# Kernel tuning notes

Measured on AMD Instinct MI355X. Metric: run time of the kernel, lower is better.

The kernel has to match this reference:

```python
import jax, jax.numpy as jnp
import numpy as np

N_USERS = 100000
N_ITEMS = 40000
DIM = 64
NNZ_UI = 1500000
NNZ_II = 1000000
NNZ_UU = 1500000
UI_LAYERS = 3
ITEM_LAYERS = 2
USER_LAYERS = 2
EPS = 1e-12


def spmm(rows, cols, vals, x, n_rows):
    # sparse COO matrix (rows, cols, vals) @ dense x -> [n_rows, d]
    return jax.ops.segment_sum(vals[:, None] * x[cols], rows, num_segments=n_rows)


def l2_normalize(x):
    # matches F.normalize(x, p=2, dim=1) with eps clamp
    n = jnp.linalg.norm(x, axis=1, keepdims=True)
    return x / jnp.maximum(n, EPS)


def setup_inputs() -> dict:
    key = jax.random.key(0)
    ks = jax.random.split(key, 13)
    N = N_USERS + N_ITEMS
    return {
        "user_ui_emb": jax.random.normal(ks[0], (N_USERS, DIM), jnp.float32) * 0.1,
        "item_ui_emb": jax.random.normal(ks[1], (N_ITEMS, DIM), jnp.float32) * 0.1,
        "uu_emb": jax.random.normal(ks[2], (N_USERS, DIM), jnp.float32) * 0.1,
        "ii_emb": jax.random.normal(ks[3], (N_ITEMS, DIM), jnp.float32) * 0.1,
        "ui_vals": jax.random.uniform(ks[4], (NNZ_UI,), jnp.float32) / 12.0,
        "ii_vals": jax.random.uniform(ks[5], (NNZ_II,), jnp.float32) / 25.0,
        "uu_vals": jax.random.uniform(ks[6], (NNZ_UU,), jnp.float32) / 15.0,
        "ui_rows": jax.random.randint(ks[7], (NNZ_UI,), 0, N, jnp.int32),
        "ui_cols": jax.random.randint(ks[8], (NNZ_UI,), 0, N, jnp.int32),
        "ii_rows": jax.random.randint(ks[9], (NNZ_II,), 0, N_ITEMS, jnp.int32),
        "ii_cols": jax.random.randint(ks[10], (NNZ_II,), 0, N_ITEMS, jnp.int32),
        "uu_rows": jax.random.randint(ks[11], (NNZ_UU,), 0, N_USERS, jnp.int32),
        "uu_cols": jax.random.randint(ks[12], (NNZ_UU,), 0, N_USERS, jnp.int32),
    }


def reference(user_ui_emb, item_ui_emb, uu_emb, ii_emb,
              ui_vals, ii_vals, uu_vals,
              ui_rows, ui_cols, ii_rows, ii_cols, uu_rows, uu_cols):
    N = N_USERS + N_ITEMS
    # II propagation (item_loss_ratio != 0)
    ii = ii_emb
    for _ in range(ITEM_LAYERS):
        ii = spmm(ii_rows, ii_cols, ii_vals, ii, N_ITEMS)
    # UU propagation (user_loss_ratio != 0)
    uu = uu_emb
    for _ in range(USER_LAYERS):
        uu = spmm(uu_rows, uu_cols, uu_vals, uu, N_USERS)
    # LightGCN UI propagation
    ego = jnp.concatenate([user_ui_emb, item_ui_emb], axis=0)  # [N, d]
    acc = ego
    for _ in range(UI_LAYERS):
        ego = spmm(ui_rows, ui_cols, ui_vals, ego, N)
        acc = acc + ego
    all_emb = acc / (UI_LAYERS + 1)  # mean over stacked layers
    u_ui_emb = all_emb[:N_USERS]
    i_ui_emb = all_emb[N_USERS:]
    i_ui_emb = i_ui_emb + l2_normalize(ii)
    u_ui_emb = u_ui_emb + l2_normalize(uu)
    return (u_ui_emb, i_ui_emb, ii, uu)
```

## Files before the change

### kernel.cpp

```cpp
#include <hip/hip_runtime.h>

#define N_USERS_C 100000
#define N_ITEMS_C 40000
#define NTOT_C    140000
#define DIM_C     64

__device__ __forceinline__ unsigned short f2bf(float f) {
    unsigned u = __float_as_uint(f);
    unsigned r = (u + 0x7FFFu + ((u >> 16) & 1u)) >> 16;
    return (unsigned short)r;
}
__device__ __forceinline__ float bf2f(unsigned short h) {
    return __uint_as_float((unsigned)h << 16);
}


template <int LOG_BR>
__global__ __launch_bounds__(256) void bucket_hist(
    const int* __restrict__ rows, int* __restrict__ bkt_count, int nnz, int NB) {
    __shared__ int cnt[256];
    if (threadIdx.x < NB) cnt[threadIdx.x] = 0;
    __syncthreads();
    for (int e = blockIdx.x * 256 + threadIdx.x; e < nnz; e += gridDim.x * 256)
        atomicAdd(&cnt[rows[e] >> LOG_BR], 1);
    __syncthreads();
    if (threadIdx.x < NB) {
        int c = cnt[threadIdx.x];
        if (c) atomicAdd(&bkt_count[threadIdx.x], c);
    }
}

__global__ __launch_bounds__(256) void bucket_scan(
    const int* __restrict__ bkt_count, int* __restrict__ bkt_start,
    int* __restrict__ bkt_cursor, int NB, int nnz) {
    __shared__ int s[256];
    int v = (threadIdx.x < NB) ? bkt_count[threadIdx.x] : 0;
    s[threadIdx.x] = v;
    __syncthreads();
    #pragma unroll
    for (int off = 1; off < 256; off <<= 1) {
        int t = (threadIdx.x >= off) ? s[threadIdx.x - off] : 0;
        __syncthreads();
        s[threadIdx.x] += t;
        __syncthreads();
    }
    if (threadIdx.x < NB) {
        int ex = s[threadIdx.x] - v;
        bkt_start[threadIdx.x] = ex;
        bkt_cursor[threadIdx.x] = ex;
    }
    if (threadIdx.x == 0) bkt_start[NB] = nnz;
}

template <int LOG_BR>
__global__ __launch_bounds__(256) void partition_edges(
    const int* __restrict__ rows, const int* __restrict__ cols,
    const float* __restrict__ vals, int* __restrict__ bkt_cursor,
    int2* __restrict__ inter, int nnz) {
    __shared__ int cnt[256];
    __shared__ int base[256];
    const int tile = blockIdx.x * 4096;
    cnt[threadIdx.x] = 0;
    __syncthreads();
    int myrow[16];
    #pragma unroll
    for (int i = 0; i < 16; ++i) {
        int e = tile + i * 256 + threadIdx.x;
        int r = (e < nnz) ? rows[e] : -1;
        myrow[i] = r;
        if (r >= 0) atomicAdd(&cnt[r >> LOG_BR], 1);
    }
    __syncthreads();
    {
        int c = cnt[threadIdx.x];
        if (c) base[threadIdx.x] = atomicAdd(&bkt_cursor[threadIdx.x], c);
        cnt[threadIdx.x] = 0;
    }
    __syncthreads();
    #pragma unroll
    for (int i = 0; i < 16; ++i) {
        int r = myrow[i];
        if (r < 0) continue;
        int b = r >> LOG_BR;
        int rank = atomicAdd(&cnt[b], 1);
        int e = tile + i * 256 + threadIdx.x;
        int rl = r & ((1 << LOG_BR) - 1);
        inter[base[b] + rank] = make_int2((rl << 18) | cols[e],
                                          __float_as_int(vals[e]));
    }
}

template <int LOG_BR>
__global__ __launch_bounds__(256) void bucket_to_csr(
    const int* __restrict__ bkt_start, const int2* __restrict__ inter,
    int2* __restrict__ spack, int* __restrict__ rowptr, int n_rows, int nnz) {
    const int BR = 1 << LOG_BR;
    const int C = BR / 256;
    __shared__ int hist[BR];
    __shared__ int bsum[256];
    const int b = blockIdx.x;
    const int lo = bkt_start[b], hi = bkt_start[b + 1];
    #pragma unroll
    for (int j = 0; j < C; ++j) hist[threadIdx.x * C + j] = 0;
    __syncthreads();
    for (int i = lo + threadIdx.x; i < hi; i += 256)
        atomicAdd(&hist[inter[i].x >> 18], 1);
    __syncthreads();
    int loc[4];
    int sum = 0;
    #pragma unroll
    for (int j = 0; j < C; ++j) { loc[j] = sum; sum += hist[threadIdx.x * C + j]; }
    bsum[threadIdx.x] = sum;
    __syncthreads();
    #pragma unroll
    for (int off = 1; off < 256; off <<= 1) {
        int t = (threadIdx.x >= off) ? bsum[threadIdx.x - off] : 0;
        __syncthreads();
        bsum[threadIdx.x] += t;
        __syncthreads();
    }
    int texcl = bsum[threadIdx.x] - sum;
    __syncthreads();
    #pragma unroll
    for (int j = 0; j < C; ++j) {
        int r = threadIdx.x * C + j;
        int abs0 = lo + texcl + loc[j];
        int grow = (b << LOG_BR) + r;
        if (grow < n_rows) rowptr[grow] = abs0;
        hist[r] = abs0;
    }
    if (b == gridDim.x - 1 && threadIdx.x == 0) rowptr[n_rows] = nnz;
    __syncthreads();
    for (int i = lo + threadIdx.x; i < hi; i += 256) {
        int2 p = inter[i];
        int pos = atomicAdd(&hist[p.x >> 18], 1);
        spack[pos] = make_int2(p.x & 0x3FFFF, p.y);
    }
}

__global__ __launch_bounds__(256) void to_bf16(
    const float* __restrict__ src, unsigned short* __restrict__ dst, int n4) {
    int gid = blockIdx.x * blockDim.x + threadIdx.x;
    if (gid >= n4) return;
    float4 v = ((const float4*)src)[gid];
    ushort4 o;
    o.x = f2bf(v.x); o.y = f2bf(v.y); o.z = f2bf(v.z); o.w = f2bf(v.w);
    ((ushort4*)dst)[gid] = o;
}

__global__ __launch_bounds__(256) void concat_to_bf16(
    const float* __restrict__ user_ui, const float* __restrict__ item_ui,
    unsigned short* __restrict__ dst) {
    int gid = blockIdx.x * blockDim.x + threadIdx.x;
    const int n4u = N_USERS_C * DIM_C / 4;
    const int n4  = NTOT_C * DIM_C / 4;
    if (gid >= n4) return;
    float4 v = (gid < n4u) ? ((const float4*)user_ui)[gid]
                           : ((const float4*)item_ui)[gid - n4u];
    ushort4 o;
    o.x = f2bf(v.x); o.y = f2bf(v.y); o.z = f2bf(v.z); o.w = f2bf(v.w);
    ((ushort4*)dst)[gid] = o;
}

template <int MODE>
__global__ __launch_bounds__(256) void spmm_csr2(
    const int* __restrict__ rowptr, const int2* __restrict__ spack,
    const unsigned short* __restrict__ x, unsigned short* __restrict__ out_bf,
    float* __restrict__ out_f32, float* __restrict__ acc,
    const float* __restrict__ ego_u, const float* __restrict__ ego_i,
    int n_rows, int nnz) {
    const int wpair = (blockIdx.x * 256 + threadIdx.x) >> 6;
    const int lane  = threadIdx.x & 63;
    const int l     = lane & 31;
    const int row   = wpair * 2 + (lane >> 5);

    int j = rowptr[row];
    int e = rowptr[row + 1];
    int rem = e - j;
    int orem = __shfl_xor(rem, 32, 64);
    int mrem = rem > orem ? rem : orem;

    const unsigned* __restrict__ xw = (const unsigned*)x;
    const int last = nnz - 1;

    float s0x = 0.f, s0y = 0.f, s1x = 0.f, s1y = 0.f;
    float s2x = 0.f, s2y = 0.f, s3x = 0.f, s3y = 0.f;

    if (mrem > 0) {
        int base = j;
        int2 p0 = spack[min(base + 0, last)];
        int2 p1 = spack[min(base + 1, last)];
        int2 p2 = spack[min(base + 2, last)];
        int2 p3 = spack[min(base + 3, last)];
        for (;;) {
            unsigned g0 = xw[(0 < rem) ? ((p0.x << 5) + l) : l];
            unsigned g1 = xw[(1 < rem) ? ((p1.x << 5) + l) : l];
            unsigned g2 = xw[(2 < rem) ? ((p2.x << 5) + l) : l];
            unsigned g3 = xw[(3 < rem) ? ((p3.x << 5) + l) : l];
            int nb = base + 4;
            int2 q0 = spack[min(nb + 0, last)];
            int2 q1 = spack[min(nb + 1, last)];
            int2 q2 = spack[min(nb + 2, last)];
            int2 q3 = spack[min(nb + 3, last)];
            float v0 = (0 < rem) ? __int_as_float(p0.y) : 0.f;
            float v1 = (1 < rem) ? __int_as_float(p1.y) : 0.f;
            float v2 = (2 < rem) ? __int_as_float(p2.y) : 0.f;
            float v3 = (3 < rem) ? __int_as_float(p3.y) : 0.f;
            s0x += v0 * __uint_as_float(g0 << 16);
            s0y += v0 * __uint_as_float(g0 & 0xFFFF0000u);
            s1x += v1 * __uint_as_float(g1 << 16);
            s1y += v1 * __uint_as_float(g1 & 0xFFFF0000u);
            s2x += v2 * __uint_as_float(g2 << 16);
            s2y += v2 * __uint_as_float(g2 & 0xFFFF0000u);
            s3x += v3 * __uint_as_float(g3 << 16);
            s3y += v3 * __uint_as_float(g3 & 0xFFFF0000u);
            mrem -= 4;
            if (mrem <= 0) break;
            rem -= 4;
            base = nb;
            p0 = q0; p1 = q1; p2 = q2; p3 = q3;
        }
    }
    float sx = (s0x + s1x) + (s2x + s3x);
    float sy = (s0y + s1y) + (s2y + s3y);

    const size_t idx2 = (size_t)row * 32 + l;
    if (MODE == 0 || MODE == 1 || MODE == 2) {
        ushort2 o;
        o.x = f2bf(sx);
        o.y = f2bf(sy);
        ((ushort2*)out_bf)[idx2] = o;
    }
    if (MODE == 1) {
        float2 e2 = (row < N_USERS_C)
            ? ((const float2*)ego_u)[idx2]
            : ((const float2*)ego_i)[(size_t)(row - N_USERS_C) * 32 + l];
        ((float2*)acc)[idx2] = make_float2(e2.x + sx, e2.y + sy);
    } else if (MODE == 2 || MODE == 3) {
        float2 a = ((float2*)acc)[idx2];
        ((float2*)acc)[idx2] = make_float2(a.x + sx, a.y + sy);
    } else if (MODE == 4) {
        ((float2*)out_f32)[idx2] = make_float2(sx, sy);
        float ss = sx * sx + sy * sy;
        #pragma unroll
        for (int off = 1; off < 32; off <<= 1) ss += __shfl_xor(ss, off, 64);
        float denom = fmaxf(sqrtf(ss), 1e-12f);
        float2 a = ((float2*)acc)[idx2];
        a.x = a.x * 0.25f + sx / denom;
        a.y = a.y * 0.25f + sy / denom;
        ((float2*)acc)[idx2] = a;
    }
}


struct BuildWs {
    int2* spack;
    int2* inter;
    int* rowptr;
    int* bkt_count;
    int* bkt_start;
    int* bkt_cursor;
};

template <int LOG_BR>
static inline void build_csr(const int* rows, const int* cols, const float* vals,
                             int nnz, int n_rows, const BuildWs& W, hipStream_t s) {
    const int NB = (n_rows + (1 << LOG_BR) - 1) >> LOG_BR;
    hipMemsetAsync(W.bkt_count, 0, (size_t)NB * sizeof(int), s);
    bucket_hist<LOG_BR><<<512, 256, 0, s>>>(rows, W.bkt_count, nnz, NB);
    bucket_scan<<<1, 256, 0, s>>>(W.bkt_count, W.bkt_start, W.bkt_cursor, NB, nnz);
    int p1b = (nnz + 4095) / 4096;
    partition_edges<LOG_BR><<<p1b, 256, 0, s>>>(rows, cols, vals, W.bkt_cursor,
                                                W.inter, nnz);
    bucket_to_csr<LOG_BR><<<NB, 256, 0, s>>>(W.bkt_start, W.inter, W.spack,
                                             W.rowptr, n_rows, nnz);
}

template <int MODE>
static inline void run_spmm(const int* rowptr, const int2* spack,
                            const unsigned short* x, unsigned short* out_bf,
                            float* out_f32, float* acc, const float* ego_u,
                            const float* ego_i, int n_rows, int nnz, hipStream_t s) {
    int blocks = (n_rows * 32 + 255) / 256;
    spmm_csr2<MODE><<<blocks, 256, 0, s>>>(rowptr, spack, x, out_bf, out_f32,
                                           acc, ego_u, ego_i, n_rows, nnz);
}

extern "C" void kernel_launch(void* const* d_in, const int* in_sizes, int n_in,
                              void* d_out, int out_size, void* d_ws, size_t ws_size,
                              hipStream_t stream) {
    const float* user_ui = (const float*)d_in[0];
    const float* item_ui = (const float*)d_in[1];
    const float* uu_emb  = (const float*)d_in[2];
    const float* ii_emb  = (const float*)d_in[3];
    const float* ui_vals = (const float*)d_in[4];
    const float* ii_vals = (const float*)d_in[5];
    const float* uu_vals = (const float*)d_in[6];
    const int* ui_rows = (const int*)d_in[7];
    const int* ui_cols = (const int*)d_in[8];
    const int* ii_rows = (const int*)d_in[9];
    const int* ii_cols = (const int*)d_in[10];
    const int* uu_rows = (const int*)d_in[11];
    const int* uu_cols = (const int*)d_in[12];
    const int nnz_ui = in_sizes[4];
    const int nnz_ii = in_sizes[5];
    const int nnz_uu = in_sizes[6];
    const int max_nnz = nnz_ui > nnz_uu ? (nnz_ui > nnz_ii ? nnz_ui : nnz_ii)
                                        : (nnz_uu > nnz_ii ? nnz_uu : nnz_ii);

    float* out    = (float*)d_out;
    float* acc    = out;
    float* acc_u  = acc;
    float* acc_i  = acc + (size_t)N_USERS_C * DIM_C;
    float* out_ii = out + (size_t)NTOT_C * DIM_C;
    float* out_uu = out_ii + (size_t)N_ITEMS_C * DIM_C;

    char* p = (char*)d_ws;
    BuildWs W;
    W.spack = (int2*)p;                         p += (size_t)max_nnz * sizeof(int2);
    unsigned short* buf0 = (unsigned short*)p;
    W.inter = (int2*)p;                         p += (size_t)NTOT_C * DIM_C * sizeof(unsigned short);
    unsigned short* buf1 = (unsigned short*)p;  p += (size_t)NTOT_C * DIM_C * sizeof(unsigned short);
    W.rowptr     = (int*)p;                     p += (size_t)(NTOT_C + 1) * sizeof(int);
    W.bkt_count  = (int*)p;                     p += 257 * sizeof(int);
    W.bkt_start  = (int*)p;                     p += 258 * sizeof(int);
    W.bkt_cursor = (int*)p;                     p += 257 * sizeof(int);

    build_csr<10>(ui_rows, ui_cols, ui_vals, nnz_ui, NTOT_C, W, stream);
    {
        int n4 = NTOT_C * DIM_C / 4;
        concat_to_bf16<<<(n4 + 255) / 256, 256, 0, stream>>>(user_ui, item_ui, buf1);
    }
    run_spmm<1>(W.rowptr, W.spack, buf1, buf0, nullptr, acc, user_ui, item_ui,
                NTOT_C, nnz_ui, stream);
    run_spmm<2>(W.rowptr, W.spack, buf0, buf1, nullptr, acc, nullptr, nullptr,
                NTOT_C, nnz_ui, stream);
    run_spmm<3>(W.rowptr, W.spack, buf1, nullptr, nullptr, acc, nullptr, nullptr,
                NTOT_C, nnz_ui, stream);

    build_csr<8>(ii_rows, ii_cols, ii_vals, nnz_ii, N_ITEMS_C, W, stream);
    {
        int n4 = N_ITEMS_C * DIM_C / 4;
        to_bf16<<<(n4 + 255) / 256, 256, 0, stream>>>(ii_emb, buf0, n4);
    }
    run_spmm<0>(W.rowptr, W.spack, buf0, buf1, nullptr, nullptr, nullptr, nullptr,
                N_ITEMS_C, nnz_ii, stream);
    run_spmm<4>(W.rowptr, W.spack, buf1, nullptr, out_ii, acc_i, nullptr, nullptr,
                N_ITEMS_C, nnz_ii, stream);

    build_csr<9>(uu_rows, uu_cols, uu_vals, nnz_uu, N_USERS_C, W, stream);
    {
        int n4 = N_USERS_C * DIM_C / 4;
        to_bf16<<<(n4 + 255) / 256, 256, 0, stream>>>(uu_emb, buf0, n4);
    }
    run_spmm<0>(W.rowptr, W.spack, buf0, buf1, nullptr, nullptr, nullptr, nullptr,
                N_USERS_C, nnz_uu, stream);
    run_spmm<4>(W.rowptr, W.spack, buf1, nullptr, out_uu, acc_u, nullptr, nullptr,
                N_USERS_C, nnz_uu, stream);
}
```

Before: 712.1 us.

## Batch II and UU graphs into one block-diagonal CSR; use quarter-wave rows

The separate item-item and user-user propagations are merged into one block-diagonal sparse matrix over a concatenated embedding, with row and column offsets applied during partitioning. This halves the number of CSR builds and SpMM launches for those graphs, and MODE 5 remaps rows back into the accumulator. The SpMM kernel also changes from 32 lanes per row with 2 bf16 values each to 16 lanes per row with 4 values each, so a wave handles 4 rows and issues wider gathers. The fallback keeps the separate path when the workspace is too small, and the grid size now assumes n_rows is divisible by 16.

```diff
diff --git a/kernel.cpp b/kernel.cpp
--- a/kernel.cpp
+++ b/kernel.cpp
@@ -10,19 +10,17 @@
     unsigned r = (u + 0x7FFFu + ((u >> 16) & 1u)) >> 16;
     return (unsigned short)r;
 }
-__device__ __forceinline__ float bf2f(unsigned short h) {
-    return __uint_as_float((unsigned)h << 16);
-}
 
 
 template <int LOG_BR>
 __global__ __launch_bounds__(256) void bucket_hist(
-    const int* __restrict__ rows, int* __restrict__ bkt_count, int nnz, int NB) {
+    const int* __restrict__ rows, int row_off, int* __restrict__ bkt_count,
+    int nnz, int NB) {
     __shared__ int cnt[256];
     if (threadIdx.x < NB) cnt[threadIdx.x] = 0;
     __syncthreads();
     for (int e = blockIdx.x * 256 + threadIdx.x; e < nnz; e += gridDim.x * 256)
-        atomicAdd(&cnt[rows[e] >> LOG_BR], 1);
+        atomicAdd(&cnt[(rows[e] + row_off) >> LOG_BR], 1);
     __syncthreads();
     if (threadIdx.x < NB) {
         int c = cnt[threadIdx.x];
@@ -55,8 +53,8 @@
 template <int LOG_BR>
 __global__ __launch_bounds__(256) void partition_edges(
     const int* __restrict__ rows, const int* __restrict__ cols,
-    const float* __restrict__ vals, int* __restrict__ bkt_cursor,
-    int2* __restrict__ inter, int nnz) {
+    const float* __restrict__ vals, int row_off, int col_off,
+    int* __restrict__ bkt_cursor, int2* __restrict__ inter, int nnz) {
     __shared__ int cnt[256];
     __shared__ int base[256];
     const int tile = blockIdx.x * 4096;
@@ -66,7 +64,7 @@
     #pragma unroll
     for (int i = 0; i < 16; ++i) {
         int e = tile + i * 256 + threadIdx.x;
-        int r = (e < nnz) ? rows[e] : -1;
+        int r = (e < nnz) ? (rows[e] + row_off) : -1;
         myrow[i] = r;
         if (r >= 0) atomicAdd(&cnt[r >> LOG_BR], 1);
     }
@@ -85,7 +83,7 @@
         int rank = atomicAdd(&cnt[b], 1);
         int e = tile + i * 256 + threadIdx.x;
         int rl = r & ((1 << LOG_BR) - 1);
-        inter[base[b] + rank] = make_int2((rl << 18) | cols[e],
+        inter[base[b] + rank] = make_int2((rl << 18) | (cols[e] + col_off),
                                           __float_as_int(vals[e]));
     }
 }
@@ -138,152 +136,122 @@
     }
 }
 
-__global__ __launch_bounds__(256) void to_bf16(
-    const float* __restrict__ src, unsigned short* __restrict__ dst, int n4) {
+__global__ __launch_bounds__(256) void concat2_to_bf16(
+    const float* __restrict__ A, const float* __restrict__ B, int n4A,
+    int n4tot, unsigned short* __restrict__ dst) {
     int gid = blockIdx.x * blockDim.x + threadIdx.x;
-    if (gid >= n4) return;
-    float4 v = ((const float4*)src)[gid];
+    if (gid >= n4tot) return;
+    float4 v = (gid < n4A) ? ((const float4*)A)[gid] : ((const float4*)B)[gid - n4A];
     ushort4 o;
     o.x = f2bf(v.x); o.y = f2bf(v.y); o.z = f2bf(v.z); o.w = f2bf(v.w);
     ((ushort4*)dst)[gid] = o;
 }
 
-__global__ __launch_bounds__(256) void concat_to_bf16(
-    const float* __restrict__ user_ui, const float* __restrict__ item_ui,
-    unsigned short* __restrict__ dst) {
-    int gid = blockIdx.x * blockDim.x + threadIdx.x;
-    const int n4u = N_USERS_C * DIM_C / 4;
-    const int n4  = NTOT_C * DIM_C / 4;
-    if (gid >= n4) return;
-    float4 v = (gid < n4u) ? ((const float4*)user_ui)[gid]
-                           : ((const float4*)item_ui)[gid - n4u];
-    ushort4 o;
-    o.x = f2bf(v.x); o.y = f2bf(v.y); o.z = f2bf(v.z); o.w = f2bf(v.w);
-    ((ushort4*)dst)[gid] = o;
-}
-
 template <int MODE>
-__global__ __launch_bounds__(256) void spmm_csr2(
+__global__ __launch_bounds__(256) void spmm_csr4(
     const int* __restrict__ rowptr, const int2* __restrict__ spack,
     const unsigned short* __restrict__ x, unsigned short* __restrict__ out_bf,
     float* __restrict__ out_f32, float* __restrict__ acc,
     const float* __restrict__ ego_u, const float* __restrict__ ego_i,
     int n_rows, int nnz) {
-    const int wpair = (blockIdx.x * 256 + threadIdx.x) >> 6;
-    const int lane  = threadIdx.x & 63;
-    const int l     = lane & 31;
-    const int row   = wpair * 2 + (lane >> 5);
+    const int wq   = (blockIdx.x * 256 + threadIdx.x) >> 6;
+    const int lane = threadIdx.x & 63;
+    const int l    = lane & 15;
+    const int row  = wq * 4 + (lane >> 4);
 
     int j = rowptr[row];
     int e = rowptr[row + 1];
     int rem = e - j;
-    int orem = __shfl_xor(rem, 32, 64);
-    int mrem = rem > orem ? rem : orem;
-
-    const unsigned* __restrict__ xw = (const unsigned*)x;
+    int m1 = max(rem, __shfl_xor(rem, 16, 64));
+    int mrem = max(m1, __shfl_xor(m1, 32, 64));
+
+    const uint2* __restrict__ xq = (const uint2*)x;
     const int last = nnz - 1;
 
-    float s0x = 0.f, s0y = 0.f, s1x = 0.f, s1y = 0.f;
-    float s2x = 0.f, s2y = 0.f, s3x = 0.f, s3y = 0.f;
+    float4 sa[4];
+    #pragma unroll
+    for (int u = 0; u < 4; ++u) sa[u] = make_float4(0.f, 0.f, 0.f, 0.f);
 
     if (mrem > 0) {
         int base = j;
-        int2 p0 = spack[min(base + 0, last)];
-        int2 p1 = spack[min(base + 1, last)];
-        int2 p2 = spack[min(base + 2, last)];
-        int2 p3 = spack[min(base + 3, last)];
+        int2 p[4];
+        #pragma unroll
+        for (int u = 0; u < 4; ++u) p[u] = spack[min(base + u, last)];
         for (;;) {
-            unsigned g0 = xw[(0 < rem) ? ((p0.x << 5) + l) : l];
-            unsigned g1 = xw[(1 < rem) ? ((p1.x << 5) + l) : l];
-            unsigned g2 = xw[(2 < rem) ? ((p2.x << 5) + l) : l];
-            unsigned g3 = xw[(3 < rem) ? ((p3.x << 5) + l) : l];
+            uint2 g[4];
+            #pragma unroll
+            for (int u = 0; u < 4; ++u)
+                g[u] = xq[(u < rem) ? ((p[u].x << 4) + l) : l];
             int nb = base + 4;
-            int2 q0 = spack[min(nb + 0, last)];
-            int2 q1 = spack[min(nb + 1, last)];
-            int2 q2 = spack[min(nb + 2, last)];
-            int2 q3 = spack[min(nb + 3, last)];
-            float v0 = (0 < rem) ? __int_as_float(p0.y) : 0.f;
-            float v1 = (1 < rem) ? __int_as_float(p1.y) : 0.f;
-            float v2 = (2 < rem) ? __int_as_float(p2.y) : 0.f;
-            float v3 = (3 < rem) ? __int_as_float(p3.y) : 0.f;
-            s0x += v0 * __uint_as_float(g0 << 16);
-            s0y += v0 * __uint_as_float(g0 & 0xFFFF0000u);
-            s1x += v1 * __uint_as_float(g1 << 16);
-            s1y += v1 * __uint_as_float(g1 & 0xFFFF0000u);
-            s2x += v2 * __uint_as_float(g2 << 16);
-            s2y += v2 * __uint_as_float(g2 & 0xFFFF0000u);
-            s3x += v3 * __uint_as_float(g3 << 16);
-            s3y += v3 * __uint_as_float(g3 & 0xFFFF0000u);
+            int2 q[4];
+            #pragma unroll
+            for (int u = 0; u < 4; ++u) q[u] = spack[min(nb + u, last)];
+            #pragma unroll
+            for (int u = 0; u < 4; ++u) {
+                float v = (u < rem) ? __int_as_float(p[u].y) : 0.f;
+                sa[u].x += v * __uint_as_float(g[u].x << 16);
+                sa[u].y += v * __uint_as_float(g[u].x & 0xFFFF0000u);
+                sa[u].z += v * __uint_as_float(g[u].y << 16);
+                sa[u].w += v * __uint_as_float(g[u].y & 0xFFFF0000u);
+            }
             mrem -= 4;
             if (mrem <= 0) break;
             rem -= 4;
             base = nb;
-            p0 = q0; p1 = q1; p2 = q2; p3 = q3;
+            #pragma unroll
+            for (int u = 0; u < 4; ++u) p[u] = q[u];
         }
     }
-    float sx = (s0x + s1x) + (s2x + s3x);
-    float sy = (s0y + s1y) + (s2y + s3y);
-
-    const size_t idx2 = (size_t)row * 32 + l;
+    float4 s;
+    s.x = (sa[0].x + sa[1].x) + (sa[2].x + sa[3].x);
+    s.y = (sa[0].y + sa[1].y) + (sa[2].y + sa[3].y);
+    s.z = (sa[0].z + sa[1].z) + (sa[2].z + sa[3].z);
+    s.w = (sa[0].w + sa[1].w) + (sa[2].w + sa[3].w);
+
+    const size_t idx4 = (size_t)row * 16 + l;
     if (MODE == 0 || MODE == 1 || MODE == 2) {
-        ushort2 o;
-        o.x = f2bf(sx);
-        o.y = f2bf(sy);
-        ((ushort2*)out_bf)[idx2] = o;
+        ushort4 o;
+        o.x = f2bf(s.x); o.y = f2bf(s.y); o.z = f2bf(s.z); o.w = f2bf(s.w);
+        ((ushort4*)out_bf)[idx4] = o;
     }
     if (MODE == 1) {
-        float2 e2 = (row < N_USERS_C)
-            ? ((const float2*)ego_u)[idx2]
-            : ((const float2*)ego_i)[(size_t)(row - N_USERS_C) * 32 + l];
-        ((float2*)acc)[idx2] = make_float2(e2.x + sx, e2.y + sy);
+        float4 e4 = (row < N_USERS_C)
+            ? ((const float4*)ego_u)[idx4]
+            : ((const float4*)ego_i)[(size_t)(row - N_USERS_C) * 16 + l];
+        ((float4*)acc)[idx4] = make_float4(e4.x + s.x, e4.y + s.y,
+                                           e4.z + s.z, e4.w + s.w);
     } else if (MODE == 2 || MODE == 3) {
-        float2 a = ((float2*)acc)[idx2];
-        ((float2*)acc)[idx2] = make_float2(a.x + sx, a.y + sy);
-    } else if (MODE == 4) {
-        ((float2*)out_f32)[idx2] = make_float2(sx, sy);
-        float ss = sx * sx + sy * sy;
+        float4 a = ((const float4*)acc)[idx4];
+        ((float4*)acc)[idx4] = make_float4(a.x + s.x, a.y + s.y,
+                                           a.z + s.z, a.w + s.w);
+    } else if (MODE == 4 || MODE == 5) {
+        ((float4*)out_f32)[idx4] = s;
+        float ss = s.x * s.x + s.y * s.y + s.z * s.z + s.w * s.w;
         #pragma unroll
-        for (int off = 1; off < 32; off <<= 1) ss += __shfl_xor(ss, off, 64);
-        float denom = fmaxf(sqrtf(ss), 1e-12f);
-        float2 a = ((float2*)acc)[idx2];
-        a.x = a.x * 0.25f + sx / denom;
-        a.y = a.y * 0.25f + sy / denom;
-        ((float2*)acc)[idx2] = a;
-    }
-}
-
-
-struct BuildWs {
-    int2* spack;
-    int2* inter;
-    int* rowptr;
-    int* bkt_count;
-    int* bkt_start;
-    int* bkt_cursor;
-};
-
-template <int LOG_BR>
-static inline void build_csr(const int* rows, const int* cols, const float* vals,
-                             int nnz, int n_rows, const BuildWs& W, hipStream_t s) {
-    const int NB = (n_rows + (1 << LOG_BR) - 1) >> LOG_BR;
-    hipMemsetAsync(W.bkt_count, 0, (size_t)NB * sizeof(int), s);
-    bucket_hist<LOG_BR><<<512, 256, 0, s>>>(rows, W.bkt_count, nnz, NB);
-    bucket_scan<<<1, 256, 0, s>>>(W.bkt_count, W.bkt_start, W.bkt_cursor, NB, nnz);
-    int p1b = (nnz + 4095) / 4096;
-    partition_edges<LOG_BR><<<p1b, 256, 0, s>>>(rows, cols, vals, W.bkt_cursor,
-                                                W.inter, nnz);
-    bucket_to_csr<LOG_BR><<<NB, 256, 0, s>>>(W.bkt_start, W.inter, W.spack,
-                                             W.rowptr, n_rows, nnz);
-}
+        for (int off = 1; off < 16; off <<= 1) ss += __shfl_xor(ss, off, 64);
+        float inv = 1.f / fmaxf(sqrtf(ss), 1e-12f);
+        size_t aidx = idx4;
+        if (MODE == 5) {
+            int arow = (row < N_ITEMS_C) ? (N_USERS_C + row) : (row - N_ITEMS_C);
+            aidx = (size_t)arow * 16 + l;
+        }
+        float4 a = ((const float4*)acc)[aidx];
+        a.x = a.x * 0.25f + s.x * inv;
+        a.y = a.y * 0.25f + s.y * inv;
+        a.z = a.z * 0.25f + s.z * inv;
+        a.w = a.w * 0.25f + s.w * inv;
+        ((float4*)acc)[aidx] = a;
+    }
+}
+
 
 template <int MODE>
 static inline void run_spmm(const int* rowptr, const int2* spack,
                             const unsigned short* x, unsigned short* out_bf,
                             float* out_f32, float* acc, const float* ego_u,
                             const float* ego_i, int n_rows, int nnz, hipStream_t s) {
-    int blocks = (n_rows * 32 + 255) / 256;
-    spmm_csr2<MODE><<<blocks, 256, 0, s>>>(rowptr, spack, x, out_bf, out_f32,
-                                           acc, ego_u, ego_i, n_rows, nnz);
+    spmm_csr4<MODE><<<n_rows / 16, 256, 0, s>>>(rowptr, spack, x, out_bf, out_f32,
+                                                acc, ego_u, ego_i, n_rows, nnz);
 }
 
 extern "C" void kernel_launch(void* const* d_in, const int* in_sizes, int n_in,
@@ -305,8 +273,7 @@
     const int nnz_ui = in_sizes[4];
     const int nnz_ii = in_sizes[5];
     const int nnz_uu = in_sizes[6];
-    const int max_nnz = nnz_ui > nnz_uu ? (nnz_ui > nnz_ii ? nnz_ui : nnz_ii)
-                                        : (nnz_uu > nnz_ii ? nnz_uu : nnz_ii);
+    const int nnz_cat = nnz_ii + nnz_uu;
 
     float* out    = (float*)d_out;
     float* acc    = out;
@@ -314,47 +281,112 @@
     float* acc_i  = acc + (size_t)N_USERS_C * DIM_C;
     float* out_ii = out + (size_t)NTOT_C * DIM_C;
     float* out_uu = out_ii + (size_t)N_ITEMS_C * DIM_C;
+    float* out_cat = out_ii;
+
+    const size_t buf_bytes = (size_t)NTOT_C * DIM_C * sizeof(unsigned short);
+    const size_t sp_ui  = (size_t)nnz_ui * sizeof(int2);
+    const size_t sp_cat = (size_t)nnz_cat * sizeof(int2);
+    const size_t meta_bytes = ((size_t)(NTOT_C + 1) + 1024) * sizeof(int);
+
+    size_t slotA = sp_cat > sp_ui ? sp_cat : sp_ui;
+    size_t slotB = slotA > buf_bytes ? slotA : buf_bytes;
+    bool use_cat = ws_size >= slotA + slotB + buf_bytes + meta_bytes;
+    if (!use_cat) {
+        size_t mx = sp_ui;
+        if ((size_t)nnz_ii * sizeof(int2) > mx) mx = (size_t)nnz_ii * sizeof(int2);
+        if ((size_t)nnz_uu * sizeof(int2) > mx) mx = (size_t)nnz_uu * sizeof(int2);
+        slotA = mx;
+        slotB = buf_bytes;
+    }
 
     char* p = (char*)d_ws;
-    BuildWs W;
-    W.spack = (int2*)p;                         p += (size_t)max_nnz * sizeof(int2);
-    unsigned short* buf0 = (unsigned short*)p;
-    W.inter = (int2*)p;                         p += (size_t)NTOT_C * DIM_C * sizeof(unsigned short);
-    unsigned short* buf1 = (unsigned short*)p;  p += (size_t)NTOT_C * DIM_C * sizeof(unsigned short);
-    W.rowptr     = (int*)p;                     p += (size_t)(NTOT_C + 1) * sizeof(int);
-    W.bkt_count  = (int*)p;                     p += 257 * sizeof(int);
-    W.bkt_start  = (int*)p;                     p += 258 * sizeof(int);
-    W.bkt_cursor = (int*)p;                     p += 257 * sizeof(int);
-
-    build_csr<10>(ui_rows, ui_cols, ui_vals, nnz_ui, NTOT_C, W, stream);
+    int2* spack = (int2*)p;                     p += slotA;
+    int2* inter = (int2*)p;
+    unsigned short* buf0 = (unsigned short*)p;  p += slotB;
+    unsigned short* buf1 = (unsigned short*)p;  p += buf_bytes;
+    int* rowptr     = (int*)p;
+    int* bkt_count  = rowptr + (NTOT_C + 1);
+    int* bkt_start  = bkt_count + 257;
+    int* bkt_cursor = bkt_start + 258;
+
+    const int n4tot = NTOT_C * DIM_C / 4;
+    const int n4u   = N_USERS_C * DIM_C / 4;
+    const int n4i   = N_ITEMS_C * DIM_C / 4;
+
     {
-        int n4 = NTOT_C * DIM_C / 4;
-        concat_to_bf16<<<(n4 + 255) / 256, 256, 0, stream>>>(user_ui, item_ui, buf1);
-    }
-    run_spmm<1>(W.rowptr, W.spack, buf1, buf0, nullptr, acc, user_ui, item_ui,
+        const int NB = (NTOT_C + 1023) >> 10;
+        hipMemsetAsync(bkt_count, 0, (size_t)NB * sizeof(int), stream);
+        bucket_hist<10><<<512, 256, 0, stream>>>(ui_rows, 0, bkt_count, nnz_ui, NB);
+        bucket_scan<<<1, 256, 0, stream>>>(bkt_count, bkt_start, bkt_cursor, NB, nnz_ui);
+        partition_edges<10><<<(nnz_ui + 4095) / 4096, 256, 0, stream>>>(
+            ui_rows, ui_cols, ui_vals, 0, 0, bkt_cursor, inter, nnz_ui);
+        bucket_to_csr<10><<<NB, 256, 0, stream>>>(bkt_start, inter, spack, rowptr,
+                                                  NTOT_C, nnz_ui);
+    }
+    concat2_to_bf16<<<(n4tot + 255) / 256, 256, 0, stream>>>(user_ui, item_ui,
+                                                             n4u, n4tot, buf1);
+    run_spmm<1>(rowptr, spack, buf1, buf0, nullptr, acc, user_ui, item_ui,
                 NTOT_C, nnz_ui, stream);
-    run_spmm<2>(W.rowptr, W.spack, buf0, buf1, nullptr, acc, nullptr, nullptr,
+    run_spmm<2>(rowptr, spack, buf0, buf1, nullptr, acc, nullptr, nullptr,
                 NTOT_C, nnz_ui, stream);
-    run_spmm<3>(W.rowptr, W.spack, buf1, nullptr, nullptr, acc, nullptr, nullptr,
+    run_spmm<3>(rowptr, spack, buf1, nullptr, nullptr, acc, nullptr, nullptr,
                 NTOT_C, nnz_ui, stream);
 
-    build_csr<8>(ii_rows, ii_cols, ii_vals, nnz_ii, N_ITEMS_C, W, stream);
-    {
-        int n4 = N_ITEMS_C * DIM_C / 4;
-        to_bf16<<<(n4 + 255) / 256, 256, 0, stream>>>(ii_emb, buf0, n4);
-    }
-    run_spmm<0>(W.rowptr, W.spack, buf0, buf1, nullptr, nullptr, nullptr, nullptr,
-                N_ITEMS_C, nnz_ii, stream);
-    run_spmm<4>(W.rowptr, W.spack, buf1, nullptr, out_ii, acc_i, nullptr, nullptr,
-                N_ITEMS_C, nnz_ii, stream);
-
-    build_csr<9>(uu_rows, uu_cols, uu_vals, nnz_uu, N_USERS_C, W, stream);
-    {
-        int n4 = N_USERS_C * DIM_C / 4;
-        to_bf16<<<(n4 + 255) / 256, 256, 0, stream>>>(uu_emb, buf0, n4);
-    }
-    run_spmm<0>(W.rowptr, W.spack, buf0, buf1, nullptr, nullptr, nullptr, nullptr,
-                N_USERS_C, nnz_uu, stream);
-    run_spmm<4>(W.rowptr, W.spack, buf1, nullptr, out_uu, acc_u, nullptr, nullptr,
-                N_USERS_C, nnz_uu, stream);
-}
+    if (use_cat) {
+        const int NB = (NTOT_C + 1023) >> 10;
+        hipMemsetAsync(bkt_count, 0, (size_t)NB * sizeof(int), stream);
+        bucket_hist<10><<<512, 256, 0, stream>>>(ii_rows, 0, bkt_count, nnz_ii, NB);
+        bucket_hist<10><<<512, 256, 0, stream>>>(uu_rows, N_ITEMS_C, bkt_count,
+                                                 nnz_uu, NB);
+        bucket_scan<<<1, 256, 0, stream>>>(bkt_count, bkt_start, bkt_cursor, NB,
+                                           nnz_cat);
+        partition_edges<10><<<(nnz_ii + 4095) / 4096, 256, 0, stream>>>(
+            ii_rows, ii_cols, ii_vals, 0, 0, bkt_cursor, inter, nnz_ii);
+        partition_edges<10><<<(nnz_uu + 4095) / 4096, 256, 0, stream>>>(
+            uu_rows, uu_cols, uu_vals, N_ITEMS_C, N_ITEMS_C, bkt_cursor, inter,
+            nnz_uu);
+        bucket_to_csr<10><<<NB, 256, 0, stream>>>(bkt_start, inter, spack, rowptr,
+                                                  NTOT_C, nnz_cat);
+        concat2_to_bf16<<<(n4tot + 255) / 256, 256, 0, stream>>>(ii_emb, uu_emb,
+                                                                 n4i, n4tot, buf1);
+        run_spmm<0>(rowptr, spack, buf1, buf0, nullptr, nullptr, nullptr, nullptr,
+                    NTOT_C, nnz_cat, stream);
+        run_spmm<5>(rowptr, spack, buf0, nullptr, out_cat, acc, nullptr, nullptr,
+                    NTOT_C, nnz_cat, stream);
+    } else {
+        {
+            const int NB = (N_ITEMS_C + 255) >> 8;
+            hipMemsetAsync(bkt_count, 0, (size_t)NB * sizeof(int), stream);
+            bucket_hist<8><<<512, 256, 0, stream>>>(ii_rows, 0, bkt_count, nnz_ii, NB);
+            bucket_scan<<<1, 256, 0, stream>>>(bkt_count, bkt_start, bkt_cursor,
+                                               NB, nnz_ii);
+            partition_edges<8><<<(nnz_ii + 4095) / 4096, 256, 0, stream>>>(
+                ii_rows, ii_cols, ii_vals, 0, 0, bkt_cursor, inter, nnz_ii);
+            bucket_to_csr<8><<<NB, 256, 0, stream>>>(bkt_start, inter, spack,
+                                                     rowptr, N_ITEMS_C, nnz_ii);
+        }
+        concat2_to_bf16<<<(n4i + 255) / 256, 256, 0, stream>>>(ii_emb, ii_emb,
+                                                               n4i, n4i, buf0);
+        run_spmm<0>(rowptr, spack, buf0, buf1, nullptr, nullptr, nullptr, nullptr,
+                    N_ITEMS_C, nnz_ii, stream);
+        run_spmm<4>(rowptr, spack, buf1, nullptr, out_ii, acc_i, nullptr, nullptr,
+                    N_ITEMS_C, nnz_ii, stream);
+        {
+            const int NB = (N_USERS_C + 511) >> 9;
+            hipMemsetAsync(bkt_count, 0, (size_t)NB * sizeof(int), stream);
+            bucket_hist<9><<<512, 256, 0, stream>>>(uu_rows, 0, bkt_count, nnz_uu, NB);
+            bucket_scan<<<1, 256, 0, stream>>>(bkt_count, bkt_start, bkt_cursor,
+                                               NB, nnz_uu);
+            partition_edges<9><<<(nnz_uu + 4095) / 4096, 256, 0, stream>>>(
+                uu_rows, uu_cols, uu_vals, 0, 0, bkt_cursor, inter, nnz_uu);
+            bucket_to_csr<9><<<NB, 256, 0, stream>>>(bkt_start, inter, spack,
+                                                     rowptr, N_USERS_C, nnz_uu);
+        }
+        concat2_to_bf16<<<(n4u + 255) / 256, 256, 0, stream>>>(uu_emb, uu_emb,
+                                                               n4u, n4u, buf0);
+        run_spmm<0>(rowptr, spack, buf0, buf1, nullptr, nullptr, nullptr, nullptr,
+                    N_USERS_C, nnz_uu, stream);
+        run_spmm<4>(rowptr, spack, buf1, nullptr, out_uu, acc_u, nullptr, nullptr,
+                    N_USERS_C, nnz_uu, stream);
+    }
+}
```

After: 641.1 us. 1.11x faster.
